# Kernel optimization log

Measured on AMD Instinct MI355X. Metric: run time of the kernel, lower is better.

The kernel has to match this reference:

```python
import jax, jax.numpy as jnp
import numpy as np


def setup_inputs() -> dict:
    key = jax.random.key(0)
    k1, k2 = jax.random.split(key)
    x = jax.random.normal(k1, (32, 128, 112, 112), dtype=jnp.float32)
    weight = jax.random.normal(k2, (256, 128, 3, 3), dtype=jnp.float32)
    return {"x": x, "weight": weight}


def reference(x, weight):
    # Equivalent to torch unfold + einsum: valid (no padding), stride-1
    # cross-correlation conv2d with no bias.
    # x: [B, Cin, H, W], weight: [Cout, Cin, kh, kw] -> [B, Cout, H-kh+1, W-kw+1]
    return jax.lax.conv_general_dilated(
        x, weight,
        window_strides=(1, 1),
        padding="VALID",
        dimension_numbers=("NCHW", "OIHW", "NCHW"),
    )
```

## Files before the change

### kernel.cpp

```cpp
#include <hip/hip_runtime.h>

typedef __attribute__((ext_vector_type(8))) short short8;
typedef __attribute__((ext_vector_type(4))) float f32x4;
typedef unsigned int u32;

#define CIN   128
#define COUT  256
#define H     112
#define W     112
#define OH    110
#define OW    110
#define KHW   9
#define TH    8
#define TW    32
#define IHH   10
#define IWW   34
#define NPIX  340
#define XB    (NPIX*8*16)
#define WB    16384

__device__ __forceinline__ short f2b(float f) {
  unsigned u = __builtin_bit_cast(unsigned, f);
  unsigned r = (u + 0x7FFFu + ((u >> 16) & 1u)) >> 16;
  return (short)r;
}

__device__ __forceinline__ void gload16(const void* g, void* l) {
  __builtin_amdgcn_global_load_lds(
      (const __attribute__((address_space(1))) u32*)g,
      (__attribute__((address_space(3))) u32*)l, 16, 0, 0);
}


template<bool XT, bool WT>
__global__ __launch_bounds__(512, 4)
void conv_main(const float* __restrict__ x, const float* __restrict__ wgt,
               const short* __restrict__ wt, const short* __restrict__ xt,
               const short* __restrict__ zp, float* __restrict__ out) {
  __shared__ __align__(16) char smem[XB + 2*WB];
  char* sx = smem;
  char* sw = smem + XB;

  const int tid = threadIdx.x;

  const int nb  = gridDim.x;
  const int swz = (blockIdx.x & 7) * (nb >> 3) + (blockIdx.x >> 3);
  const int b    = swz / 112;
  const int rem  = swz - b * 112;
  const int cblk = rem / 56;
  const int rem2 = rem - cblk * 56;
  const int t_w  = rem2 / 14;
  const int t_h  = rem2 - t_w * 14;
  const int h0 = t_h * TH, w0 = t_w * TW;

  auto stage_x = [&](int hh) {
    if (XT) {
      const short* xtb = xt + (size_t)b * (H*W*CIN);
      #pragma unroll
      for (int it = 0; it < 6; ++it) {
        int u = it*512 + tid;
        if (u < 8*NPIX) {
          int p = u >> 3;
          int Geff = (u & 7) ^ (p & 7);
          int iy = p / IWW, ix = p - iy * IWW;
          int gy = h0 + iy, gx = w0 + ix;
          const short* src = (gy < H && gx < W)
              ? xtb + ((size_t)gy*W + gx)*CIN + hh*64 + Geff*8
              : zp;
          gload16(src, sx + u*16);
        }
      }
    } else {
      const float* xh = x + (size_t)b * CIN * (H*W) + (size_t)(hh*64) * (H*W);
      for (int u = tid; u < 8 * NPIX; u += 512) {
        int G = u / NPIX, p = u - G * NPIX;
        int iy = p / IWW, ix = p - iy * IWW;
        int gy = h0 + iy, gx = w0 + ix;
        short8 v = {0,0,0,0,0,0,0,0};
        if (gy < H && gx < W) {
          const float* s = xh + (size_t)(G*8) * (H*W) + gy * W + gx;
          #pragma unroll
          for (int j = 0; j < 8; ++j) v[j] = f2b(s[j * (H*W)]);
        }
        *(short8*)(sx + p*128 + ((G ^ (p & 7)) << 4)) = v;
      }
    }
  };

  auto stage_w = [&](int st, int buf) {
    int hh = st / 9, tap = st - hh * 9;
    if (WT) {
      const short* base = wt + (size_t)tap * (COUT*CIN)
                             + (size_t)(cblk*128) * CIN + hh * 64;
      #pragma unroll
      for (int it = 0; it < 2; ++it) {
        int slot = it * 512 + tid;
        int c = slot >> 3, gsw = (slot & 7) ^ (c & 7);
        gload16(base + c * CIN + gsw * 8, sw + buf*WB + slot * 16);
      }
    } else {
      #pragma unroll
      for (int it = 0; it < 2; ++it) {
        int slot = it * 512 + tid;
        int c = slot >> 3, gsw = (slot & 7) ^ (c & 7);
        int cout = cblk*128 + c;
        short8 v;
        #pragma unroll
        for (int j = 0; j < 8; ++j) {
          int cin = hh*64 + gsw*8 + j;
          v[j] = f2b(wgt[cout*(CIN*KHW) + cin*KHW + tap]);
        }
        *(short8*)(sw + buf*WB + slot * 16) = v;
      }
    }
  };

  const int lane = tid & 63;
  const int wid  = tid >> 6;
  const int wm = wid >> 2;
  const int wn = wid & 3;
  const int l15 = lane & 15;
  const int kgrp = lane >> 4;

  f32x4 acc[4][4] = {};

  stage_x(0);
  stage_w(0, 0);
  __syncthreads();

  for (int st = 0; st < 18; ++st) {
    if (st + 1 < 18) stage_w(st + 1, (st + 1) & 1);

    const int tap = st % 9;
    const int kh = tap / 3, kw = tap - (tap/3)*3;
    const char* swb = sw + (st & 1) * WB;

    #pragma unroll
    for (int s = 0; s < 2; ++s) {
      const int g = s*4 + kgrp;
      const int aslot = (g ^ (l15 & 7)) << 4;
      short8 a[4];
      #pragma unroll
      for (int mi = 0; mi < 4; ++mi)
        a[mi] = *(const short8*)(swb + (wm*64 + mi*16 + l15) * 128 + aslot);
      short8 bf[4];
      #pragma unroll
      for (int ni = 0; ni < 4; ++ni) {
        int p = (2*wn + (ni >> 1) + kh) * IWW + (ni & 1)*16 + l15 + kw;
        bf[ni] = *(const short8*)(sx + p*128 + ((g ^ (p & 7)) << 4));
      }
      #pragma unroll
      for (int mi = 0; mi < 4; ++mi)
        #pragma unroll
        for (int ni = 0; ni < 4; ++ni)
          acc[mi][ni] = __builtin_amdgcn_mfma_f32_16x16x32_bf16(a[mi], bf[ni], acc[mi][ni], 0, 0, 0);
    }

    if (st == 8) {
      __syncthreads();
      stage_x(1);
      __syncthreads();
    } else {
      __syncthreads();
    }
  }

  float* ob = out + (size_t)b * COUT * (OH*OW);
  #pragma unroll
  for (int ni = 0; ni < 4; ++ni) {
    int oh = h0 + 2*wn + (ni >> 1);
    int ow = w0 + (ni & 1)*16 + l15;
    if (oh < OH && ow < OW) {
      #pragma unroll
      for (int mi = 0; mi < 4; ++mi) {
        #pragma unroll
        for (int r = 0; r < 4; ++r) {
          int cout = cblk*128 + wm*64 + mi*16 + kgrp*4 + r;
          ob[(size_t)cout*(OH*OW) + oh*OW + ow] = acc[mi][ni][r];
        }
      }
    }
  }
}

__global__ void wprep(const float* __restrict__ wgt, short* __restrict__ wt,
                      short* __restrict__ zp) {
  int idx = blockIdx.x * 256 + threadIdx.x;
  if (idx < 128) zp[idx] = 0;
  if (idx >= KHW*COUT*CIN) return;
  int khw  = idx / (COUT*CIN);
  int rem  = idx - khw*(COUT*CIN);
  int cout = rem >> 7, cin = rem & 127;
  wt[idx] = f2b(wgt[cout*(CIN*KHW) + cin*KHW + khw]);
}

__global__ __launch_bounds__(256)
void xprep(const float* __restrict__ x, short* __restrict__ xt) {
  __shared__ short lsh[CIN * 113];
  const int bh = blockIdx.x;
  const int b = bh / H, h = bh - b * H;
  const float* src = x + ((size_t)b * CIN * H + h) * W;
  for (int u = threadIdx.x; u < CIN * W; u += 256) {
    int c = u / W, w = u - c * W;
    lsh[c * 113 + w] = f2b(src[(size_t)c * (H*W) + w]);
  }
  __syncthreads();
  short* dst = xt + (size_t)bh * (W * CIN);
  for (int o = threadIdx.x; o < W * CIN / 8; o += 256) {
    int w = o >> 4, s = o & 15;
    short8 v;
    #pragma unroll
    for (int j = 0; j < 8; ++j) v[j] = lsh[(s*8 + j) * 113 + w];
    *(short8*)(dst + o * 8) = v;
  }
}

extern "C" void kernel_launch(void* const* d_in, const int* in_sizes, int n_in,
                              void* d_out, int out_size, void* d_ws, size_t ws_size,
                              hipStream_t stream) {
  const float* x   = (const float*)d_in[0];
  const float* wgt = (const float*)d_in[1];
  float* out = (float*)d_out;
  const size_t wt_bytes = (size_t)(KHW*COUT*CIN) * sizeof(short);
  const size_t zp_bytes = 256;
  const size_t xt_bytes = (size_t)32 * H * W * CIN * sizeof(short);
  dim3 grid(3584);
  if (ws_size >= wt_bytes + zp_bytes + xt_bytes) {
    short* wt = (short*)d_ws;
    short* zp = (short*)((char*)d_ws + wt_bytes);
    short* xt = (short*)((char*)d_ws + wt_bytes + zp_bytes);
    wprep<<<(KHW*COUT*CIN + 255)/256, 256, 0, stream>>>(wgt, wt, zp);
    xprep<<<32 * H, 256, 0, stream>>>(x, xt);
    conv_main<true, true><<<grid, 512, 0, stream>>>(x, wgt, wt, xt, zp, out);
  } else if (ws_size >= wt_bytes + zp_bytes) {
    short* wt = (short*)d_ws;
    short* zp = (short*)((char*)d_ws + wt_bytes);
    wprep<<<(KHW*COUT*CIN + 255)/256, 256, 0, stream>>>(wgt, wt, zp);
    conv_main<false, true><<<grid, 512, 0, stream>>>(x, wgt, wt, nullptr, zp, out);
  } else {
    conv_main<false, false><<<grid, 512, 0, stream>>>(x, wgt, nullptr, nullptr, nullptr, out);
  }
}
```

Baseline: 356.4 us.

## Switch inner GEMM to 32x32x16 bf16 MFMA with software-pipelined fragment loads

Replaces the 4x4 grid of 16x16x32 MFMAs per wave with a 2x2 grid of 32x32x16 MFMAs, covering the same 64x64 output tile per wave with fewer, larger instructions and fewer LDS fragment reads. The K loop is split into four 16-wide steps with double-buffered register fragments, so LDS loads for the next step are issued before the current MFMAs. The epilogue remaps accumulator rows to the 32x32 output layout. The larger MFMA shape changes register layout and LDS access patterns, which may affect bank conflicts and store coalescing.

```diff
diff --git a/kernel.cpp b/kernel.cpp
--- a/kernel.cpp
+++ b/kernel.cpp
@@ -1,7 +1,7 @@
 #include <hip/hip_runtime.h>
 
 typedef __attribute__((ext_vector_type(8))) short short8;
-typedef __attribute__((ext_vector_type(4))) float f32x4;
+typedef __attribute__((ext_vector_type(16))) float f32x16;
 typedef unsigned int u32;
 
 #define CIN   128
@@ -119,10 +119,10 @@
   const int wid  = tid >> 6;
   const int wm = wid >> 2;
   const int wn = wid & 3;
-  const int l15 = lane & 15;
-  const int kgrp = lane >> 4;
-
-  f32x4 acc[4][4] = {};
+  const int l31 = lane & 31;
+  const int lh  = lane >> 5;
+
+  f32x16 acc[2][2] = {};
 
   stage_x(0);
   stage_w(0, 0);
@@ -135,26 +135,37 @@
     const int kh = tap / 3, kw = tap - (tap/3)*3;
     const char* swb = sw + (st & 1) * WB;
 
-    #pragma unroll
-    for (int s = 0; s < 2; ++s) {
-      const int g = s*4 + kgrp;
-      const int aslot = (g ^ (l15 & 7)) << 4;
-      short8 a[4];
-      #pragma unroll
-      for (int mi = 0; mi < 4; ++mi)
-        a[mi] = *(const short8*)(swb + (wm*64 + mi*16 + l15) * 128 + aslot);
-      short8 bf[4];
-      #pragma unroll
-      for (int ni = 0; ni < 4; ++ni) {
-        int p = (2*wn + (ni >> 1) + kh) * IWW + (ni & 1)*16 + l15 + kw;
-        bf[ni] = *(const short8*)(sx + p*128 + ((g ^ (p & 7)) << 4));
-      }
-      #pragma unroll
-      for (int mi = 0; mi < 4; ++mi)
+    const char* aptr0 = swb + (wm*64 + l31) * 128;
+    const int   asw   = l31 & 7;
+    const int   prow0 = (2*wn + kh) * IWW + l31 + kw;
+    const int   prow1 = prow0 + IWW;
+
+    short8 aA[2], bA[2], aB[2], bB[2];
+    auto LDF = [&](int ks, short8* av, short8* bv) {
+      const int g = ks*2 + lh;
+      const int aslot = (g ^ asw) << 4;
+      av[0] = *(const short8*)(aptr0 + aslot);
+      av[1] = *(const short8*)(aptr0 + 32*128 + aslot);
+      bv[0] = *(const short8*)(sx + prow0*128 + ((g ^ (prow0 & 7)) << 4));
+      bv[1] = *(const short8*)(sx + prow1*128 + ((g ^ (prow1 & 7)) << 4));
+    };
+    auto MF = [&](short8* av, short8* bv) {
+      #pragma unroll
+      for (int mi = 0; mi < 2; ++mi)
         #pragma unroll
-        for (int ni = 0; ni < 4; ++ni)
-          acc[mi][ni] = __builtin_amdgcn_mfma_f32_16x16x32_bf16(a[mi], bf[ni], acc[mi][ni], 0, 0, 0);
-    }
+        for (int ni = 0; ni < 2; ++ni)
+          acc[mi][ni] = __builtin_amdgcn_mfma_f32_32x32x16_bf16(
+              av[mi], bv[ni], acc[mi][ni], 0, 0, 0);
+    };
+
+    LDF(0, aA, bA);
+    LDF(1, aB, bB);
+    MF(aA, bA);
+    LDF(2, aA, bA);
+    MF(aB, bB);
+    LDF(3, aB, bB);
+    MF(aA, bA);
+    MF(aB, bB);
 
     if (st == 8) {
       __syncthreads();
@@ -167,15 +178,16 @@
 
   float* ob = out + (size_t)b * COUT * (OH*OW);
   #pragma unroll
-  for (int ni = 0; ni < 4; ++ni) {
-    int oh = h0 + 2*wn + (ni >> 1);
-    int ow = w0 + (ni & 1)*16 + l15;
+  for (int ni = 0; ni < 2; ++ni) {
+    int oh = h0 + 2*wn + ni;
+    int ow = w0 + l31;
     if (oh < OH && ow < OW) {
       #pragma unroll
-      for (int mi = 0; mi < 4; ++mi) {
+      for (int mi = 0; mi < 2; ++mi) {
         #pragma unroll
-        for (int r = 0; r < 4; ++r) {
-          int cout = cblk*128 + wm*64 + mi*16 + kgrp*4 + r;
+        for (int r = 0; r < 16; ++r) {
+          int crow = (r & 3) + 8*(r >> 2) + 4*lh;
+          int cout = cblk*128 + wm*64 + mi*32 + crow;
           ob[(size_t)cout*(OH*OW) + oh*OW + ow] = acc[mi][ni][r];
         }
       }
```

Result: slower. 487.7 us (+36.8%).
